# Kernel tuning notes

Hardware: AMD Instinct MI355X
Metric: run time of the kernel (lower is better)

The kernel has to match this reference:

```python
import jax, jax.numpy as jnp
import numpy as np

B, N, C, K = 8, 4096, 128, 20  # batch, points-per-cloud, channels (n_cout), knn neighbors
NEG_SLOPE = 0.01  # torch F.leaky_relu default


def setup_inputs() -> dict:
    key = jax.random.key(0)
    ks = jax.random.split(key, 6)
    s = 1.0 / np.sqrt(C).astype(np.float32)
    xyz = jax.random.normal(ks[0], (B, 3, N), jnp.float32)
    points = jax.random.normal(ks[1], (B, C, N), jnp.float32)
    Wc = jax.random.normal(ks[2], (C, C), jnp.float32) * s  # center 1x1 conv weight (out,in)
    bc = jax.random.normal(ks[3], (C,), jnp.float32) * s
    Wg = jax.random.normal(ks[4], (C, C), jnp.float32) * s  # grouped 1x1 conv weight
    bg = jax.random.normal(ks[5], (C,), jnp.float32) * s
    return {"xyz": xyz, "points": points, "Wc": Wc, "bc": bc, "Wg": Wg, "bg": bg}


def reference(xyz, points, Wc, bc, Wg, bg):
    # xyz: [B,3,N], points: [B,C,N]
    k = K
    shortcut = points
    p = jax.nn.leaky_relu(points, NEG_SLOPE)        # [B,C,N]
    pt = jnp.transpose(p, (0, 2, 1))                # [B,N,C]
    xt = jnp.transpose(xyz, (0, 2, 1))              # [B,N,3]

    # pairwise squared distances [B,N,N]
    sq_norm = jnp.sum(xt * xt, axis=-1)             # [B,N]
    sq = sq_norm[:, :, None] - 2.0 * jnp.einsum('bnd,bmd->bnm', xt, xt) + sq_norm[:, None, :]

    # knn: k+1 nearest (incl. self), drop self -> [B,N,k]
    _, idx = jax.lax.top_k(-sq, k + 1)
    idx = idx[:, :, 1:]

    # gather neighbor features: [B,N,k,C]
    grouped = jax.vmap(lambda a, i: a[i])(pt, idx)

    # center 1x1 conv on [B,C,1,N] == per-point linear
    center = jnp.einsum('oc,bcn->bon', Wc, p) + bc[None, :, None]      # [B,C,N]
    # grouped 1x1 conv on [B,C,k,N]
    gout = jnp.einsum('oc,bnkc->bokn', Wg, grouped) + bg[None, :, None, None]  # [B,C,k,N]

    # mean over concat([center(1), grouped(k)], axis=2) then residual
    pooled = (center + jnp.sum(gout, axis=2)) / (k + 1)
    return pooled + shortcut
```

## Files before the change

kernel.cpp:

```cpp
#include <hip/hip_runtime.h>

#define B 8
#define N 4096
#define C 128
#define C2 256
#define KNN 21
#define CAP 22

typedef unsigned long long u64;
typedef unsigned int u32;
typedef unsigned short u16;

typedef __attribute__((ext_vector_type(8))) short bf16x8;
typedef __attribute__((ext_vector_type(4))) float f32x4;

__device__ __forceinline__ float bf2f(u16 u) {
    return __uint_as_float(((u32)u) << 16);
}
__device__ __forceinline__ u16 f2bf(float f) {
    u32 x = __float_as_uint(f);
    return (u16)((x + 0x7FFFu + ((x >> 16) & 1u)) >> 16);
}

__global__ __launch_bounds__(256) void k_transpose_lrelu(
        const float* __restrict__ pts, u16* __restrict__ X) {
    __shared__ u16 tile[32][33];
    int b  = blockIdx.z;
    int c0 = blockIdx.y * 32;
    int n0 = blockIdx.x * 32;
    int tx = threadIdx.x, ty = threadIdx.y;
    const float* src = pts + (size_t)b * C * N;
    #pragma unroll
    for (int i = 0; i < 32; i += 8) {
        float v = src[(size_t)(c0 + ty + i) * N + n0 + tx];
        if (v < 0.f) v = __fmul_rn(v, 0.01f);
        tile[ty + i][tx] = f2bf(v);
    }
    __syncthreads();
    u16* dst = X + (size_t)b * N * C2;
    #pragma unroll
    for (int i = 0; i < 32; i += 8) {
        dst[(size_t)(n0 + ty + i) * C2 + (c0 + tx)] = tile[tx][ty + i];
    }
}

__global__ __launch_bounds__(256) void k_knn_gather(
        const float* __restrict__ xyz, u16* __restrict__ X) {
    __shared__ __align__(16) char lds[50176];
    float4* stg  = (float4*)lds;
    u32*    kbuf = (u32*)(lds + 16384);
    u16*    ibuf = (u16*)(lds + 16384 + 22528);
    u64*    mg   = (u64*)lds;
    __shared__ u16 win[64 * KNN];

    int tid = threadIdx.x;
    int w = tid >> 6, l = tid & 63;
    int b = blockIdx.y;
    int n0 = blockIdx.x * 64;
    int nq = n0 + l;

    const float* xz = xyz + (size_t)b * 3 * N;
    float qx = xz[nq], qy = xz[N + nq], qz = xz[2 * N + nq];
    float snq = __fadd_rn(__fadd_rn(__fmul_rn(qx, qx), __fmul_rn(qy, qy)),
                          __fmul_rn(qz, qz));

    u32 key[KNN], idx[KNN];
    #pragma unroll
    for (int i = 0; i < KNN; ++i) { key[i] = 0xFFFFFFFFu; idx[i] = 0u; }
    int cnt = 0;
    u32 thr = 0xFFFFFFFFu;
    float4* mystg = stg + w * 256;

    auto compact = [&]() {
        #pragma unroll 1
        for (int i = 0; i < CAP; ++i) {
            if (__ballot(i < cnt) == 0ull) break;
            u32 kv = kbuf[i * 256 + tid];
            u32 iv = ibuf[i * 256 + tid];
            bool ins = (i < cnt) && (kv < key[20]);
            if (__ballot(ins) != 0ull) {
                key[20] = ins ? kv : key[20];
                idx[20] = ins ? iv : idx[20];
                #pragma unroll
                for (int t = 19; t >= 0; --t) {
                    bool sw = key[t] > key[t + 1];
                    u32 ka = sw ? key[t + 1] : key[t];
                    u32 kz = sw ? key[t] : key[t + 1];
                    u32 ia = sw ? idx[t + 1] : idx[t];
                    u32 iz = sw ? idx[t] : idx[t + 1];
                    key[t] = ka; key[t + 1] = kz;
                    idx[t] = ia; idx[t + 1] = iz;
                }
            }
        }
        cnt = 0;
        thr = key[20];
    };

    for (int sc = 0; sc < 4; ++sc) {
        int m0 = w * 1024 + sc * 256;
        #pragma unroll
        for (int r = 0; r < 4; ++r) {
            int j = l + 64 * r, m = m0 + j;
            float x = xz[m], y = xz[N + m], z = xz[2 * N + m];
            float sn = __fadd_rn(__fadd_rn(__fmul_rn(x, x), __fmul_rn(y, y)),
                                 __fmul_rn(z, z));
            mystg[j] = make_float4(x, y, z, sn);
        }
        asm volatile("s_waitcnt lgkmcnt(0)" ::: "memory");
        for (int cc = 0; cc < 256; cc += 8) {
            #pragma unroll
            for (int j = 0; j < 8; ++j) {
                float4 cp = mystg[cc + j];
                int m = m0 + cc + j;
                float dot = __fadd_rn(__fadd_rn(__fmul_rn(qx, cp.x),
                                                __fmul_rn(qy, cp.y)),
                                      __fmul_rn(qz, cp.z));
                float sq = __fadd_rn(__fsub_rn(snq, __fadd_rn(dot, dot)), cp.w);
                u32 bits = __float_as_uint(sq);
                u32 kb = bits ^ (0x80000000u | (u32)(((int)bits) >> 31));
                kbuf[cnt * 256 + tid] = kb;
                ibuf[cnt * 256 + tid] = (u16)m;
                cnt += (kb < thr);
            }
            if (__ballot(cnt >= 15) != 0ull) compact();
        }
    }
    compact();

    __syncthreads();
    #pragma unroll
    for (int j = 0; j < KNN; ++j)
        mg[(w * 64 + l) * KNN + j] = ((u64)key[j] << 32) | (u64)idx[j];
    __syncthreads();

    if (w == 0) {
        int p0 = 0, p1 = 0, p2 = 0, p3 = 0;
        for (int j = 0; j < KNN; ++j) {
            u64 c0 = mg[(0 * 64 + l) * KNN + p0];
            u64 c1 = mg[(1 * 64 + l) * KNN + p1];
            u64 c2 = mg[(2 * 64 + l) * KNN + p2];
            u64 c3 = mg[(3 * 64 + l) * KNN + p3];
            u64 m01 = c0 < c1 ? c0 : c1; int s01 = c0 < c1 ? 0 : 1;
            u64 m23 = c2 < c3 ? c2 : c3; int s23 = c2 < c3 ? 2 : 3;
            u64 mm = m01 < m23 ? m01 : m23;
            int sel = m01 < m23 ? s01 : s23;
            win[l * KNN + j] = (u16)(mm & 0xFFFFu);
            p0 += (sel == 0); p1 += (sel == 1); p2 += (sel == 2); p3 += (sel == 3);
        }
    }
    __syncthreads();

    const u16* Xb = X + (size_t)b * N * C2;
    for (int qq = 0; qq < 16; ++qq) {
        int q = w * 16 + qq;
        float f0 = 0.f, f1 = 0.f;
        #pragma unroll
        for (int j = 1; j < KNN; ++j) {
            int m = win[q * KNN + j];
            u32 u2 = *(const u32*)(Xb + (size_t)m * C2 + 2 * l);
            f0 += bf2f((u16)(u2 & 0xFFFFu));
            f1 += bf2f((u16)(u2 >> 16));
        }
        u16* dst = X + ((size_t)b * N + n0 + q) * C2 + 128 + 2 * l;
        *(u32*)dst = ((u32)f2bf(f1) << 16) | (u32)f2bf(f0);
    }
}

__global__ __launch_bounds__(256) void k_gemm_mfma(
        const u16* __restrict__ X, const float* __restrict__ Wc,
        const float* __restrict__ Wg, const float* __restrict__ pts,
        const float* __restrict__ bc, const float* __restrict__ bg,
        float* __restrict__ out) {
    int wid = blockIdx.x * 4 + (threadIdx.x >> 6);
    int lane = threadIdx.x & 63;
    int ot = wid & 7;
    int nt = wid >> 3;
    int b  = nt >> 6;
    int n0 = (nt & 63) * 64;

    int l16 = lane & 15, lq = lane >> 4;
    const u16* Xb = X + (size_t)b * N * C2;
    const u16* bptr0 = Xb + (size_t)(n0 + 0 * 16 + l16) * C2 + lq * 8;
    const u16* bptr1 = Xb + (size_t)(n0 + 1 * 16 + l16) * C2 + lq * 8;
    const u16* bptr2 = Xb + (size_t)(n0 + 2 * 16 + l16) * C2 + lq * 8;
    const u16* bptr3 = Xb + (size_t)(n0 + 3 * 16 + l16) * C2 + lq * 8;
    const float* wrowc = Wc + (size_t)(ot * 16 + l16) * 128 + lq * 8;
    const float* wrowg = Wg + (size_t)(ot * 16 + l16) * 128 + lq * 8;

    f32x4 acc0 = {0.f, 0.f, 0.f, 0.f};
    f32x4 acc1 = {0.f, 0.f, 0.f, 0.f};
    f32x4 acc2 = {0.f, 0.f, 0.f, 0.f};
    f32x4 acc3 = {0.f, 0.f, 0.f, 0.f};
    #pragma unroll
    for (int kk = 0; kk < 8; ++kk) {
        const float* ws = (kk < 4) ? (wrowc + kk * 32) : (wrowg + (kk - 4) * 32);
        float4 wa = *(const float4*)ws;
        float4 wb = *(const float4*)(ws + 4);
        bf16x8 a;
        a[0] = (short)f2bf(wa.x); a[1] = (short)f2bf(wa.y);
        a[2] = (short)f2bf(wa.z); a[3] = (short)f2bf(wa.w);
        a[4] = (short)f2bf(wb.x); a[5] = (short)f2bf(wb.y);
        a[6] = (short)f2bf(wb.z); a[7] = (short)f2bf(wb.w);
        bf16x8 b0 = *(const bf16x8*)(bptr0 + kk * 32);
        bf16x8 b1 = *(const bf16x8*)(bptr1 + kk * 32);
        bf16x8 b2 = *(const bf16x8*)(bptr2 + kk * 32);
        bf16x8 b3 = *(const bf16x8*)(bptr3 + kk * 32);
        acc0 = __builtin_amdgcn_mfma_f32_16x16x32_bf16(a, b0, acc0, 0, 0, 0);
        acc1 = __builtin_amdgcn_mfma_f32_16x16x32_bf16(a, b1, acc1, 0, 0, 0);
        acc2 = __builtin_amdgcn_mfma_f32_16x16x32_bf16(a, b2, acc2, 0, 0, 0);
        acc3 = __builtin_amdgcn_mfma_f32_16x16x32_bf16(a, b3, acc3, 0, 0, 0);
    }

    const float inv21 = 1.0f / 21.0f;
    float bias[4];
    #pragma unroll
    for (int r = 0; r < 4; ++r) {
        int o = ot * 16 + lq * 4 + r;
        bias[r] = bc[o] + 20.f * bg[o];
    }
    const float* pb = pts + (size_t)b * C * N;
    float* ob = out + (size_t)b * C * N;
    f32x4 accs[4] = {acc0, acc1, acc2, acc3};
    #pragma unroll
    for (int t = 0; t < 4; ++t) {
        int n = n0 + t * 16 + l16;
        #pragma unroll
        for (int r = 0; r < 4; ++r) {
            int o = ot * 16 + lq * 4 + r;
            ob[(size_t)o * N + n] =
                (accs[t][r] + bias[r]) * inv21 + pb[(size_t)o * N + n];
        }
    }
}

extern "C" void kernel_launch(void* const* d_in, const int* in_sizes, int n_in,
                              void* d_out, int out_size, void* d_ws, size_t ws_size,
                              hipStream_t stream) {
    const float* xyz = (const float*)d_in[0];
    const float* pts = (const float*)d_in[1];
    const float* Wc  = (const float*)d_in[2];
    const float* bc  = (const float*)d_in[3];
    const float* Wg  = (const float*)d_in[4];
    const float* bg  = (const float*)d_in[5];
    float* out = (float*)d_out;

    u16* X = (u16*)d_ws;

    k_transpose_lrelu<<<dim3(N / 32, C / 32, B), dim3(32, 8), 0, stream>>>(pts, X);
    k_knn_gather<<<dim3(N / 64, B), dim3(256), 0, stream>>>(xyz, X);
    k_gemm_mfma<<<dim3(1024), dim3(256), 0, stream>>>(X, Wc, Wg, pts, bc, bg, out);
}
```

Measured before the change: 285.4 us.

## Precompute candidate float4s globally and stream them via scalar loads in kNN

```diff
diff --git a/kernel.cpp b/kernel.cpp
--- a/kernel.cpp
+++ b/kernel.cpp
@@ -23,12 +23,23 @@
 }
 
 __global__ __launch_bounds__(256) void k_transpose_lrelu(
-        const float* __restrict__ pts, u16* __restrict__ X) {
+        const float* __restrict__ pts, u16* __restrict__ X,
+        const float* __restrict__ xyz, float4* __restrict__ cand) {
     __shared__ u16 tile[32][33];
     int b  = blockIdx.z;
     int c0 = blockIdx.y * 32;
     int n0 = blockIdx.x * 32;
     int tx = threadIdx.x, ty = threadIdx.y;
+
+    if (blockIdx.y == 0 && ty == 0) {
+        int n = n0 + tx;
+        const float* xz = xyz + (size_t)b * 3 * N;
+        float x = xz[n], y = xz[N + n], z = xz[2 * N + n];
+        float sn = __fadd_rn(__fadd_rn(__fmul_rn(x, x), __fmul_rn(y, y)),
+                             __fmul_rn(z, z));
+        cand[(size_t)b * N + n] = make_float4(x, y, z, sn);
+    }
+
     const float* src = pts + (size_t)b * C * N;
     #pragma unroll
     for (int i = 0; i < 32; i += 8) {
@@ -45,12 +56,10 @@
 }
 
 __global__ __launch_bounds__(256) void k_knn_gather(
-        const float* __restrict__ xyz, u16* __restrict__ X) {
-    __shared__ __align__(16) char lds[50176];
-    float4* stg  = (float4*)lds;
-    u32*    kbuf = (u32*)(lds + 16384);
-    u16*    ibuf = (u16*)(lds + 16384 + 22528);
-    u64*    mg   = (u64*)lds;
+        const float4* __restrict__ cand, u16* __restrict__ X) {
+    __shared__ __align__(16) char lds[45056];
+    u32* buf = (u32*)lds;
+    u64* mg  = (u64*)lds;
     __shared__ u16 win[64 * KNN];
 
     int tid = threadIdx.x;
@@ -59,33 +68,34 @@
     int n0 = blockIdx.x * 64;
     int nq = n0 + l;
 
-    const float* xz = xyz + (size_t)b * 3 * N;
-    float qx = xz[nq], qy = xz[N + nq], qz = xz[2 * N + nq];
-    float snq = __fadd_rn(__fadd_rn(__fmul_rn(qx, qx), __fmul_rn(qy, qy)),
-                          __fmul_rn(qz, qz));
-
-    u32 key[KNN], idx[KNN];
-    #pragma unroll
-    for (int i = 0; i < KNN; ++i) { key[i] = 0xFFFFFFFFu; idx[i] = 0u; }
+    const float4* candb = cand + (size_t)b * N;
+    float4 cq = candb[nq];
+    float qx = cq.x, qy = cq.y, qz = cq.z, snq = cq.w;
+
+    float key[KNN];
+    u32 idx[KNN];
+    #pragma unroll
+    for (int i = 0; i < KNN; ++i) { key[i] = __builtin_inff(); idx[i] = 0u; }
     int cnt = 0;
-    u32 thr = 0xFFFFFFFFu;
-    float4* mystg = stg + w * 256;
+    float thr = __builtin_inff();
+    u32* vb = buf + 2 * tid;
 
     auto compact = [&]() {
         #pragma unroll 1
         for (int i = 0; i < CAP; ++i) {
             if (__ballot(i < cnt) == 0ull) break;
-            u32 kv = kbuf[i * 256 + tid];
-            u32 iv = ibuf[i * 256 + tid];
+            u32 kb_ = vb[i * 512];
+            u32 ib_ = vb[i * 512 + 1];
+            float kv = __uint_as_float(kb_);
             bool ins = (i < cnt) && (kv < key[20]);
             if (__ballot(ins) != 0ull) {
                 key[20] = ins ? kv : key[20];
-                idx[20] = ins ? iv : idx[20];
+                idx[20] = ins ? ib_ : idx[20];
                 #pragma unroll
                 for (int t = 19; t >= 0; --t) {
                     bool sw = key[t] > key[t + 1];
-                    u32 ka = sw ? key[t + 1] : key[t];
-                    u32 kz = sw ? key[t] : key[t + 1];
+                    float ka = sw ? key[t + 1] : key[t];
+                    float kz = sw ? key[t] : key[t + 1];
                     u32 ia = sw ? idx[t + 1] : idx[t];
                     u32 iz = sw ? idx[t] : idx[t + 1];
                     key[t] = ka; key[t + 1] = kz;
@@ -97,41 +107,48 @@
         thr = key[20];
     };
 
-    for (int sc = 0; sc < 4; ++sc) {
-        int m0 = w * 1024 + sc * 256;
-        #pragma unroll
-        for (int r = 0; r < 4; ++r) {
-            int j = l + 64 * r, m = m0 + j;
-            float x = xz[m], y = xz[N + m], z = xz[2 * N + m];
-            float sn = __fadd_rn(__fadd_rn(__fmul_rn(x, x), __fmul_rn(y, y)),
-                                 __fmul_rn(z, z));
-            mystg[j] = make_float4(x, y, z, sn);
-        }
-        asm volatile("s_waitcnt lgkmcnt(0)" ::: "memory");
-        for (int cc = 0; cc < 256; cc += 8) {
-            #pragma unroll
-            for (int j = 0; j < 8; ++j) {
-                float4 cp = mystg[cc + j];
-                int m = m0 + cc + j;
-                float dot = __fadd_rn(__fadd_rn(__fmul_rn(qx, cp.x),
-                                                __fmul_rn(qy, cp.y)),
-                                      __fmul_rn(qz, cp.z));
-                float sq = __fadd_rn(__fsub_rn(snq, __fadd_rn(dot, dot)), cp.w);
-                u32 bits = __float_as_uint(sq);
-                u32 kb = bits ^ (0x80000000u | (u32)(((int)bits) >> 31));
-                kbuf[cnt * 256 + tid] = kb;
-                ibuf[cnt * 256 + tid] = (u16)m;
-                cnt += (kb < thr);
-            }
-            if (__ballot(cnt >= 15) != 0ull) compact();
-        }
-    }
+    auto proc1 = [&](float4 cp, int m) {
+        float dot = __fadd_rn(__fadd_rn(__fmul_rn(qx, cp.x),
+                                        __fmul_rn(qy, cp.y)),
+                              __fmul_rn(qz, cp.z));
+        float sq = __fadd_rn(__fsub_rn(snq, __fadd_rn(dot, dot)), cp.w);
+        u32* p = vb + (u32)cnt * 512;
+        p[0] = __float_as_uint(sq);
+        p[1] = (u32)m;
+        cnt += (sq < thr);
+    };
+
+    int m0 = w * 1024;
+    float4 bufA[8], bufB[8];
+#define LOADG(dst, g) do { int _b = m0 + (g) * 8;                            \
+        _Pragma("unroll")                                                    \
+        for (int _j = 0; _j < 8; ++_j) {                                     \
+            int _mu = __builtin_amdgcn_readfirstlane(_b + _j);               \
+            dst[_j] = candb[_mu];                                            \
+        } } while (0)
+
+    LOADG(bufA, 0);
+    #pragma unroll 1
+    for (int g = 0; g < 128; g += 2) {
+        LOADG(bufB, g + 1);
+        #pragma unroll
+        for (int j = 0; j < 8; ++j) proc1(bufA[j], m0 + g * 8 + j);
+        if (__ballot(cnt >= 15) != 0ull) compact();
+        if (g + 2 < 128) LOADG(bufA, g + 2);
+        #pragma unroll
+        for (int j = 0; j < 8; ++j) proc1(bufB[j], m0 + (g + 1) * 8 + j);
+        if (__ballot(cnt >= 15) != 0ull) compact();
+    }
+#undef LOADG
     compact();
 
     __syncthreads();
     #pragma unroll
-    for (int j = 0; j < KNN; ++j)
-        mg[(w * 64 + l) * KNN + j] = ((u64)key[j] << 32) | (u64)idx[j];
+    for (int j = 0; j < KNN; ++j) {
+        u32 bits = __float_as_uint(key[j]);
+        u32 kb2 = bits ^ (0x80000000u | (u32)(((int)bits) >> 31));
+        mg[(w * 64 + l) * KNN + j] = ((u64)kb2 << 32) | (u64)idx[j];
+    }
     __syncthreads();
 
     if (w == 0) {
@@ -246,8 +263,11 @@
     float* out = (float*)d_out;
 
     u16* X = (u16*)d_ws;
-
-    k_transpose_lrelu<<<dim3(N / 32, C / 32, B), dim3(32, 8), 0, stream>>>(pts, X);
-    k_knn_gather<<<dim3(N / 64, B), dim3(256), 0, stream>>>(xyz, X);
+    float4* cand = (float4*)((char*)d_ws +
+                             (size_t)B * N * C2 * sizeof(u16));
+
+    k_transpose_lrelu<<<dim3(N / 32, C / 32, B), dim3(32, 8), 0, stream>>>(
+        pts, X, xyz, cand);
+    k_knn_gather<<<dim3(N / 64, B), dim3(256), 0, stream>>>(cand, X);
     k_gemm_mfma<<<dim3(1024), dim3(256), 0, stream>>>(X, Wc, Wg, pts, bc, bg, out);
 }
```

Result: slower. 348.4 us (+22.1%).

## Precompute packed xyz+norm candidates, pad LDS staging, remap GEMM block order

Applied to the files above, without the earlier changes.

```diff
diff --git a/kernel.cpp b/kernel.cpp
--- a/kernel.cpp
+++ b/kernel.cpp
@@ -23,12 +23,23 @@
 }
 
 __global__ __launch_bounds__(256) void k_transpose_lrelu(
-        const float* __restrict__ pts, u16* __restrict__ X) {
+        const float* __restrict__ pts, u16* __restrict__ X,
+        const float* __restrict__ xyz, float4* __restrict__ cand) {
     __shared__ u16 tile[32][33];
     int b  = blockIdx.z;
     int c0 = blockIdx.y * 32;
     int n0 = blockIdx.x * 32;
     int tx = threadIdx.x, ty = threadIdx.y;
+
+    if (blockIdx.y == 0 && ty == 0) {
+        int n = n0 + tx;
+        const float* xz = xyz + (size_t)b * 3 * N;
+        float x = xz[n], y = xz[N + n], z = xz[2 * N + n];
+        float sn = __fadd_rn(__fadd_rn(__fmul_rn(x, x), __fmul_rn(y, y)),
+                             __fmul_rn(z, z));
+        cand[(size_t)b * N + n] = make_float4(x, y, z, sn);
+    }
+
     const float* src = pts + (size_t)b * C * N;
     #pragma unroll
     for (int i = 0; i < 32; i += 8) {
@@ -45,11 +56,11 @@
 }
 
 __global__ __launch_bounds__(256) void k_knn_gather(
-        const float* __restrict__ xyz, u16* __restrict__ X) {
-    __shared__ __align__(16) char lds[50176];
+        const float4* __restrict__ cand, u16* __restrict__ X) {
+    __shared__ __align__(16) char lds[52224];
     float4* stg  = (float4*)lds;
-    u32*    kbuf = (u32*)(lds + 16384);
-    u16*    ibuf = (u16*)(lds + 16384 + 22528);
+    u32*    kbuf = (u32*)(lds + 18432);
+    u16*    ibuf = (u16*)(lds + 18432 + 22528);
     u64*    mg   = (u64*)lds;
     __shared__ u16 win[64 * KNN];
 
@@ -59,17 +70,15 @@
     int n0 = blockIdx.x * 64;
     int nq = n0 + l;
 
-    const float* xz = xyz + (size_t)b * 3 * N;
-    float qx = xz[nq], qy = xz[N + nq], qz = xz[2 * N + nq];
-    float snq = __fadd_rn(__fadd_rn(__fmul_rn(qx, qx), __fmul_rn(qy, qy)),
-                          __fmul_rn(qz, qz));
+    const float4* candb = cand + (size_t)b * N;
+    float4 cq = candb[nq];
+    float qx = cq.x, qy = cq.y, qz = cq.z, snq = cq.w;
 
     u32 key[KNN], idx[KNN];
     #pragma unroll
     for (int i = 0; i < KNN; ++i) { key[i] = 0xFFFFFFFFu; idx[i] = 0u; }
     int cnt = 0;
     u32 thr = 0xFFFFFFFFu;
-    float4* mystg = stg + w * 256;
 
     auto compact = [&]() {
         #pragma unroll 1
@@ -97,21 +106,25 @@
         thr = key[20];
     };
 
+    float4* mystg = stg + w * 288;
+    int wl = l + (l >> 3);
+
     for (int sc = 0; sc < 4; ++sc) {
         int m0 = w * 1024 + sc * 256;
-        #pragma unroll
-        for (int r = 0; r < 4; ++r) {
-            int j = l + 64 * r, m = m0 + j;
-            float x = xz[m], y = xz[N + m], z = xz[2 * N + m];
-            float sn = __fadd_rn(__fadd_rn(__fmul_rn(x, x), __fmul_rn(y, y)),
-                                 __fmul_rn(z, z));
-            mystg[j] = make_float4(x, y, z, sn);
-        }
+        float4 v0 = candb[m0 + l];
+        float4 v1 = candb[m0 + l + 64];
+        float4 v2 = candb[m0 + l + 128];
+        float4 v3 = candb[m0 + l + 192];
+        mystg[wl]       = v0;
+        mystg[wl + 72]  = v1;
+        mystg[wl + 144] = v2;
+        mystg[wl + 216] = v3;
         asm volatile("s_waitcnt lgkmcnt(0)" ::: "memory");
         for (int cc = 0; cc < 256; cc += 8) {
+            int base = cc + (cc >> 3);
             #pragma unroll
             for (int j = 0; j < 8; ++j) {
-                float4 cp = mystg[cc + j];
+                float4 cp = mystg[base + j];
                 int m = m0 + cc + j;
                 float dot = __fadd_rn(__fadd_rn(__fmul_rn(qx, cp.x),
                                                 __fmul_rn(qy, cp.y)),
@@ -172,7 +185,8 @@
         const float* __restrict__ Wg, const float* __restrict__ pts,
         const float* __restrict__ bc, const float* __restrict__ bg,
         float* __restrict__ out) {
-    int wid = blockIdx.x * 4 + (threadIdx.x >> 6);
+    int lb = (blockIdx.x & 7) * 128 + (blockIdx.x >> 3);
+    int wid = lb * 4 + (threadIdx.x >> 6);
     int lane = threadIdx.x & 63;
     int ot = wid & 7;
     int nt = wid >> 3;
@@ -246,8 +260,11 @@
     float* out = (float*)d_out;
 
     u16* X = (u16*)d_ws;
-
-    k_transpose_lrelu<<<dim3(N / 32, C / 32, B), dim3(32, 8), 0, stream>>>(pts, X);
-    k_knn_gather<<<dim3(N / 64, B), dim3(256), 0, stream>>>(xyz, X);
+    float4* cand = (float4*)((char*)d_ws +
+                             (size_t)B * N * C2 * sizeof(u16));
+
+    k_transpose_lrelu<<<dim3(N / 32, C / 32, B), dim3(32, 8), 0, stream>>>(
+        pts, X, xyz, cand);
+    k_knn_gather<<<dim3(N / 64, B), dim3(256), 0, stream>>>(cand, X);
     k_gemm_mfma<<<dim3(1024), dim3(256), 0, stream>>>(X, Wc, Wg, pts, bc, bg, out);
 }
```

New measurement: 287.4 us. About the same (+0.7%).
